# Performance work log

Measured on AMD Instinct MI355X. Metric: run time of the kernel, lower is better.

The kernel has to match this reference:

```python
import jax, jax.numpy as jnp
import numpy as np

N, E, FD, PD, C0, C1 = 50000, 1000000, 1024, 64, 64, 64


def setup_inputs() -> dict:
    key = jax.random.key(0)
    ks = iter(jax.random.split(key, 64))
    nrm = lambda s, sc=0.05: jax.random.normal(next(ks), s, jnp.float32) * sc

    def bn_p(c):
        # rows: gamma, beta, running_mean, running_var (eval-mode batchnorm)
        return jnp.stack([
            1.0 + 0.1 * jax.random.normal(next(ks), (c,)),
            0.1 * jax.random.normal(next(ks), (c,)),
            0.1 * jax.random.normal(next(ks), (c,)),
            0.5 + jax.random.uniform(next(ks), (c,)),
        ]).astype(jnp.float32)

    inp = {}
    inp["x"] = jax.random.normal(next(ks), (N, FD + 4), jnp.float32)
    inp["edge_index"] = jax.random.randint(next(ks), (2, E), 0, N, jnp.int32)
    inp["edge_attr"] = jax.random.randint(next(ks), (E,), 0, 3, jnp.int32) - 1  # {-1,0,1}
    inp["Wspf"] = nrm((PD, 4)); inp["bspf"] = nrm((PD,))
    inp["W011"] = nrm((C0, FD // 2 + PD)); inp["b011"] = nrm((C0,))
    inp["W012"] = nrm((C0, FD // 2)); inp["b012"] = nrm((C0,))
    inp["bn01"] = bn_p(C0)
    for i in (1, 2, 3):
        inp[f"e{i}W1"] = nrm((C0, 2 * C0)); inp[f"e{i}b1"] = nrm((C0,))
        inp[f"e{i}W2"] = nrm((C0, C0)); inp[f"e{i}b2"] = nrm((C0,))
        inp[f"bn1{i}"] = bn_p(C0)
    inp["s21Wl"] = nrm((C1, C0)); inp["s21bl"] = nrm((C1,)); inp["s21Wr"] = nrm((C1, C0))
    inp["bn21"] = bn_p(C1)
    for i in (1, 2, 3):
        inp[f"s3{i}Wl"] = nrm((1, C1)); inp[f"s3{i}bl"] = nrm((1,)); inp[f"s3{i}Wr"] = nrm((1, C1))
    return inp


def _bn(h, p):
    g, b, m, v = p
    return (h - m) * jax.lax.rsqrt(v + 1e-5) * g + b


def _edge_conv(h, src, dst, seg, n, W1, b1, W2, b2):
    # EdgeConv: max_j MLP([x_i, x_j - x_i]); masked edges routed to dummy segment n
    xi, xj = h[dst], h[src]
    msg = jax.nn.relu(jnp.concatenate([xi, xj - xi], axis=1) @ W1.T + b1) @ W2.T + b2
    out = jax.ops.segment_max(msg, seg, num_segments=n + 1)[:n]
    return jnp.where(jnp.isfinite(out), out, 0.0)  # nodes with no in-edges -> 0


def _sage(h, src, seg, n, Wl, bl, Wr):
    # SAGEConv: lin_l(mean_j x_j) + lin_r(x_i)
    s = jax.ops.segment_sum(h[src], seg, num_segments=n + 1)[:n]
    cnt = jax.ops.segment_sum(jnp.ones((seg.shape[0],), h.dtype), seg, num_segments=n + 1)[:n]
    agg = s / jnp.maximum(cnt, 1.0)[:, None]
    return agg @ Wl.T + bl + h @ Wr.T


def reference(x, edge_index, edge_attr, Wspf, bspf, W011, b011, W012, b012, bn01,
              e1W1, e1b1, e1W2, e1b2, bn11, e2W1, e2b1, e2W2, e2b2, bn12,
              e3W1, e3b1, e3W2, e3b2, bn13, s21Wl, s21bl, s21Wr, bn21,
              s31Wl, s31bl, s31Wr, s32Wl, s32bl, s32Wr, s33Wl, s33bl, s33Wr):
    fd = 1024
    n = x.shape[0]
    src, dst = edge_index[0], edge_index[1]
    seg1 = jnp.where(edge_attr >= 0, dst, n)  # forward-time edges
    seg2 = jnp.where(edge_attr <= 0, dst, n)  # backward-time edges
    seg3 = dst                                 # all edges

    spf = x[:, fd:fd + 4]
    x_vis = jnp.concatenate([x[:, fd // 2:fd], spf @ Wspf.T + bspf], axis=1) @ W011.T + b011
    x_aud = x[:, :fd // 2] @ W012.T + b012
    h = jax.nn.relu(_bn(x_aud + x_vis, bn01))

    def branch(eW1, eb1, eW2, eb2, bnE, seg, sWl, sbl, sWr):
        y = jax.nn.relu(_bn(_edge_conv(h, src, dst, seg, n, eW1, eb1, eW2, eb2), bnE))
        y = jax.nn.relu(_bn(_sage(y, src, seg, n, s21Wl, s21bl, s21Wr), bn21))
        return _sage(y, src, seg, n, sWl, sbl, sWr)

    o = (branch(e1W1, e1b1, e1W2, e1b2, bn11, seg1, s31Wl, s31bl, s31Wr)
         + branch(e2W1, e2b1, e2W2, e2b2, bn12, seg2, s32Wl, s32bl, s32Wr)
         + branch(e3W1, e3b1, e3W2, e3b2, bn13, seg3, s33Wl, s33bl, s33Wr))
    return jax.nn.sigmoid(o)
```

## Files before the change

### kernel.cpp

```cpp
#include <hip/hip_runtime.h>
#include <cstdint>
#include <cstddef>

#define NN 50000
#define EE 1000000
#define NBK 196
#define PW_EC 6144
#define PW_AG 8192
#define SG_PAD 136

typedef __attribute__((ext_vector_type(8))) short bf16x8;
typedef __attribute__((ext_vector_type(4))) short s16x4;
typedef __attribute__((ext_vector_type(4))) float f32x4;
typedef _Float16 f16;
typedef __attribute__((ext_vector_type(2))) _Float16 f16x2;
typedef __attribute__((ext_vector_type(4))) _Float16 f16x4;
typedef __attribute__((ext_vector_type(8))) _Float16 f16x8;

__device__ __forceinline__ void split2(float v, short& hi, short& lo) {
    union { float f; unsigned int u; } a; a.f = v;
    unsigned short h16 = (unsigned short)(a.u >> 16);
    union { unsigned int u; float f; } hf; hf.u = ((unsigned int)h16) << 16;
    union { float f; unsigned int u; } b; b.f = v - hf.f;
    hi = (short)h16;
    lo = (short)(b.u >> 16);
}

__device__ __forceinline__ f16x8 relupq(f16x8 p, f16x8 q) {
    f16x8 s = p + q;
    f16x8 z = {};
#if __has_builtin(__builtin_elementwise_max)
    return __builtin_elementwise_max(s, z);
#else
    f16x8 r;
#pragma unroll
    for (int j = 0; j < 8; j++) r[j] = (s[j] > (f16)0.f) ? s[j] : (f16)0.f;
    return r;
#endif
}

#define OFF_WHL    ((size_t)0)
#define OFF_WSPP   ((size_t)262144)
#define OFF_BIAS01 ((size_t)263168)
#define OFF_W1PQT  ((size_t)263424)
#define OFF_BIASPQ ((size_t)361728)
#define OFF_WSAGET ((size_t)363264)
#define OFF_BIAS21 ((size_t)396032)
#define OFF_BNF    ((size_t)396288)
#define OFF_W2BF   ((size_t)398848)
#define OFF_INVC4  ((size_t)423424)
#define OFF_PZ4    ((size_t)1223424)
#define OFF_RP     ((size_t)2023424)
#define OFF_PARTS  ((size_t)2223488)
#define OFF_DEG    ((size_t)2227584)
#define OFF_CNT01  ((size_t)2427648)
#define OFF_GHEAD  ((size_t)2627712)
#define OFF_SORT   ((size_t)2631808)
#define OFF_H      ((size_t)6631808)
#define OFF_PI     ((size_t)19431808)
#define OFF_QI     ((size_t)38631808)
#define OFF_Y1I    ((size_t)57831808)
#define OFF_EBUCK  OFF_H
#define OFF_AGGI   OFF_PI

__global__ __launch_bounds__(256) void k_prep(
    const float* __restrict__ Wspf, const float* __restrict__ bspf,
    const float* __restrict__ W011, const float* __restrict__ b011,
    const float* __restrict__ W012, const float* __restrict__ b012,
    const float* __restrict__ bn01,
    const float* __restrict__ e1W1, const float* __restrict__ e1b1,
    const float* __restrict__ e1b2, const float* __restrict__ bn11,
    const float* __restrict__ e2W1, const float* __restrict__ e2b1,
    const float* __restrict__ e2b2, const float* __restrict__ bn12,
    const float* __restrict__ e3W1, const float* __restrict__ e3b1,
    const float* __restrict__ e3b2, const float* __restrict__ bn13,
    const float* __restrict__ e1W2, const float* __restrict__ e2W2,
    const float* __restrict__ e3W2,
    const float* __restrict__ s21Wl, const float* __restrict__ s21bl,
    const float* __restrict__ s21Wr, const float* __restrict__ bn21,
    unsigned short* __restrict__ Whl, float* __restrict__ WspP, float* __restrict__ bias01,
    float* __restrict__ W1pqT, float* __restrict__ biasPQ,
    f16* __restrict__ Wsg16, float* __restrict__ bias21, float* __restrict__ bnf,
    f16* __restrict__ W2h)
{
    int idx = blockIdx.x * 256 + threadIdx.x;
    if (idx < 131072) {
        int hl = idx >> 16;
        int r = idx & 65535;
        int kchunk = r >> 11;
        int r2 = r & 2047;
        int blk = r2 >> 9;
        int r3 = r2 & 511;
        int lane = r3 >> 3;
        int j = r3 & 7;
        int n = lane & 15, quad = lane >> 4;
        int k = kchunk * 32 + quad * 8 + j;
        int c = blk * 16 + n;
        float s = bn01[c] * rsqrtf(bn01[192 + c] + 1e-5f);
        float w = ((k < 512) ? W012[c * 512 + k] : W011[c * 576 + (k - 512)]) * s;
        short hi, lo;
        split2(w, hi, lo);
        Whl[idx] = (unsigned short)(hl ? lo : hi);
    } else if (idx < 131072 + 24576) {
        int r = idx - 131072;
        int b = r >> 13; r &= 8191;
        int k = r >> 7, cp = r & 127;
        const float* W1 = (b == 0) ? e1W1 : (b == 1) ? e2W1 : e3W1;
        float val;
        if (cp < 64) val = W1[cp * 128 + k] - W1[cp * 128 + 64 + k];
        else         val = W1[(cp - 64) * 128 + 64 + k];
        W1pqT[b * 8192 + k * 128 + cp] = val;
    } else if (idx < 131072 + 24576 + 8192) {
        int r = idx - (131072 + 24576);
        int k = r >> 6, c = r & 63;
        float s = bn21[c] * rsqrtf(bn21[192 + c] + 1e-5f);
        float w = (k < 64) ? s21Wl[c * 64 + k] : s21Wr[c * 64 + (k - 64)];
        Wsg16[c * 128 + k] = (f16)(w * s);
    } else if (idx < 131072 + 24576 + 8192 + 64) {
        int c = idx - (131072 + 24576 + 8192);
        float s01 = bn01[c] * rsqrtf(bn01[192 + c] + 1e-5f);
        float wsp0 = 0.f, wsp1 = 0.f, wsp2 = 0.f, wsp3 = 0.f, bacc = 0.f;
        for (int j = 0; j < 64; j++) {
            float w = W011[c * 576 + 512 + j];
            wsp0 += w * Wspf[j * 4 + 0];
            wsp1 += w * Wspf[j * 4 + 1];
            wsp2 += w * Wspf[j * 4 + 2];
            wsp3 += w * Wspf[j * 4 + 3];
            bacc += w * bspf[j];
        }
        WspP[c * 4 + 0] = wsp0 * s01; WspP[c * 4 + 1] = wsp1 * s01;
        WspP[c * 4 + 2] = wsp2 * s01; WspP[c * 4 + 3] = wsp3 * s01;
        bias01[c] = (b011[c] + b012[c] + bacc) * s01 + (bn01[64 + c] - bn01[128 + c] * s01);
        float s21 = bn21[c] * rsqrtf(bn21[192 + c] + 1e-5f);
        bias21[c] = s21bl[c] * s21 + (bn21[64 + c] - bn21[128 + c] * s21);
        const float* b1a[3] = { e1b1, e2b1, e3b1 };
        const float* b2a[3] = { e1b2, e2b2, e3b2 };
        const float* bna[3] = { bn11, bn12, bn13 };
#pragma unroll
        for (int b = 0; b < 3; b++) {
            float s = bna[b][c] * rsqrtf(bna[b][192 + c] + 1e-5f);
            float tr = bna[b][64 + c] - bna[b][128 + c] * s;
            bnf[b * 192 + c] = s;
            bnf[b * 192 + 64 + c] = b2a[b][c] * s + tr;
            bnf[b * 192 + 128 + c] = tr;
            biasPQ[b * 128 + c] = b1a[b][c];
            biasPQ[b * 128 + 64 + c] = 0.f;
        }
    } else if (idx < 131072 + 24576 + 8192 + 64 + 12288) {
        int r = idx - (131072 + 24576 + 8192 + 64);
        int b = r >> 12, i = r & 4095;
        const float* W2 = (b == 0) ? e1W2 : (b == 1) ? e2W2 : e3W2;
        W2h[b * 4096 + i] = (f16)W2[i];
    }
}

__global__ __launch_bounds__(256) void k_hist(
    const int* __restrict__ dst, int* __restrict__ deg)
{
    int e = blockIdx.x * 256 + threadIdx.x;
    if (e < EE) atomicAdd(&deg[dst[e]], 1);
}

__global__ __launch_bounds__(256) void k_psum(const int* __restrict__ deg, int* __restrict__ parts)
{
    int i = blockIdx.x * 256 + threadIdx.x;
    int v = (i < NN) ? deg[i] : 0;
#pragma unroll
    for (int off = 32; off > 0; off >>= 1) v += __shfl_xor(v, off);
    __shared__ int ws4[4];
    int wid = threadIdx.x >> 6;
    if ((threadIdx.x & 63) == 0) ws4[wid] = v;
    __syncthreads();
    if (threadIdx.x == 0)
        parts[blockIdx.x] = ws4[0] + ws4[1] + ws4[2] + ws4[3];
}

__global__ __launch_bounds__(256) void k_pscan(int* __restrict__ parts, int* __restrict__ ghead)
{
    __shared__ int sbuf[256];
    int tid = threadIdx.x;
    int v = (tid < NBK) ? parts[tid] : 0;
    sbuf[tid] = v;
    __syncthreads();
    for (int off = 1; off < 256; off <<= 1) {
        int t = (tid >= off) ? sbuf[tid - off] : 0;
        __syncthreads();
        sbuf[tid] += t;
        __syncthreads();
    }
    if (tid < NBK) {
        int ex = sbuf[tid] - v;
        parts[tid] = ex;
        ghead[tid] = ex;
    }
}

__global__ __launch_bounds__(256) void k_scanfix(
    const int* __restrict__ deg, const int* __restrict__ parts, int* __restrict__ rowptr)
{
    __shared__ int sbuf[256];
    int tid = threadIdx.x;
    int i = blockIdx.x * 256 + tid;
    int v = (i < NN) ? deg[i] : 0;
    sbuf[tid] = v;
    __syncthreads();
    for (int off = 1; off < 256; off <<= 1) {
        int t = (tid >= off) ? sbuf[tid - off] : 0;
        __syncthreads();
        sbuf[tid] += t;
        __syncthreads();
    }
    int base = parts[blockIdx.x];
    if (i < NN)      rowptr[i] = base + sbuf[tid] - v;
    if (i == NN - 1) rowptr[NN] = base + sbuf[tid];
}

__global__ __launch_bounds__(256) void k_bucketA(
    const int* __restrict__ src, const int* __restrict__ dst, const int* __restrict__ attr,
    int* __restrict__ ghead, unsigned int* __restrict__ ebuck)
{
    __shared__ int hist[NBK];
    __shared__ int head[NBK];
    int tid = threadIdx.x;
    if (tid < NBK) hist[tid] = 0;
    __syncthreads();
    int base_e = blockIdx.x * 4096;
    unsigned int word[16]; int bkt[16];
#pragma unroll
    for (int k = 0; k < 16; k++) {
        int e = base_e + k * 256 + tid;
        if (e < EE) {
            int d = dst[e], s = src[e], a = attr[e] + 1;
            int b = d >> 8;
            word[k] = (unsigned)s | ((unsigned)a << 16) | ((unsigned)(d & 255) << 18);
            bkt[k] = b;
            atomicAdd(&hist[b], 1);
        } else { bkt[k] = -1; word[k] = 0; }
    }
    __syncthreads();
    if (tid < NBK) {
        int c = hist[tid];
        head[tid] = c ? atomicAdd(&ghead[tid], c) : 0;
    }
    __syncthreads();
#pragma unroll
    for (int k = 0; k < 16; k++) {
        if (bkt[k] >= 0) {
            int pos = atomicAdd(&head[bkt[k]], 1);
            ebuck[pos] = word[k];
        }
    }
}

__global__ __launch_bounds__(256) void k_bucketB(
    const int* __restrict__ rp, const unsigned int* __restrict__ ebuck,
    int* __restrict__ sorted, unsigned int* __restrict__ cnt01)
{
    __shared__ int sbuf[1024];
    __shared__ int head[1024];
    __shared__ int s2[256];
    int b = blockIdx.x, tid = threadIdx.x;
    int n0 = b * 256;
    int n1 = n0 + 256; if (n1 > NN) n1 = NN;
    int r0 = rp[n0];
    int r1 = rp[n1];
    for (int i = tid; i < 1024; i += 256) sbuf[i] = 0;
    __syncthreads();
    for (int e = r0 + tid; e < r1; e += 256)
        atomicAdd(&sbuf[(ebuck[e] >> 16) & 1023], 1);
    __syncthreads();
    int i0 = tid * 4;
    int v0 = sbuf[i0], v1 = sbuf[i0 + 1], v2 = sbuf[i0 + 2], v3 = sbuf[i0 + 3];
    if (n0 + tid < NN)
        cnt01[n0 + tid] = (unsigned)v0 | ((unsigned)v1 << 16);
    int tot = v0 + v1 + v2 + v3;
    s2[tid] = tot;
    __syncthreads();
    for (int off = 1; off < 256; off <<= 1) {
        int t = (tid >= off) ? s2[tid - off] : 0;
        __syncthreads();
        s2[tid] += t;
        __syncthreads();
    }
    int ex = s2[tid] - tot;
    head[i0]     = r0 + ex;
    head[i0 + 1] = r0 + ex + v0;
    head[i0 + 2] = r0 + ex + v0 + v1;
    head[i0 + 3] = r0 + ex + v0 + v1 + v2;
    __syncthreads();
    for (int e = r0 + tid; e < r1; e += 256) {
        unsigned int w = ebuck[e];
        int pos = atomicAdd(&head[(w >> 16) & 1023], 1);
        sorted[pos] = (int)(w & 0x3FFFFu);
    }
}

__global__ __launch_bounds__(256) void k_h(
    const float* __restrict__ x, const unsigned short* __restrict__ Whl,
    const float* __restrict__ WspP, const float* __restrict__ bias01,
    float* __restrict__ h)
{
    __shared__ unsigned short hib[2][4096];
    __shared__ unsigned short lob[2][4096];
    int tid = threadIdx.x;
    int w = tid >> 6, l = tid & 63;
    int tile = blockIdx.x;
    int m = l & 15, quad = l >> 4;
    int blk = w;
    const unsigned short* Wh = Whl;
    const unsigned short* Wl = Whl + 65536;
    const size_t xbase = (size_t)tile * 16 * 1028;

    int oct_w = l >> 1, off_w = (l & 1) * 4;

    f32x4 g[4];
#pragma unroll
    for (int p = 0; p < 4; p++)
        g[p] = *(const f32x4*)(x + xbase + (size_t)(p * 4 + w) * 1028 + l * 4);
#pragma unroll
    for (int p = 0; p < 4; p++) {
        int r = p * 4 + w;
        int op = r * 256 + (oct_w ^ (r & 7)) * 8 + off_w;
        s16x4 h4, l4;
#pragma unroll
        for (int i = 0; i < 4; i++) { short hi, lo; split2(g[p][i], hi, lo); h4[i] = hi; l4[i] = lo; }
        *(s16x4*)(&hib[0][op]) = h4;
        *(s16x4*)(&lob[0][op]) = l4;
    }
    __syncthreads();

    f32x4 acc = { 0.f, 0.f, 0.f, 0.f };
    for (int c = 0; c < 4; c++) {
        if (c < 3) {
#pragma unroll
            for (int p = 0; p < 4; p++)
                g[p] = *(const f32x4*)(x + xbase + (size_t)(p * 4 + w) * 1028 + (c + 1) * 256 + l * 4);
        }
        int buf = c & 1;
        const unsigned short* hp = &hib[buf][m * 256];
        const unsigned short* lp = &lob[buf][m * 256];
        int msw = m & 7;
#pragma unroll
        for (int ks = 0; ks < 8; ks++) {
            int oct = ks * 4 + quad;
            int ao = (oct ^ msw) * 8;
            bf16x8 xh = *(const bf16x8*)(hp + ao);
            bf16x8 xl = *(const bf16x8*)(lp + ao);
            int fb = (c * 8 + ks) * 2048 + blk * 512 + l * 8;
            bf16x8 bh = *(const bf16x8*)(Wh + fb);
            bf16x8 bl = *(const bf16x8*)(Wl + fb);
            acc = __builtin_amdgcn_mfma_f32_16x16x32_bf16(xh, bh, acc, 0, 0, 0);
            acc = __builtin_amdgcn_mfma_f32_16x16x32_bf16(xl, bh, acc, 0, 0, 0);
            acc = __builtin_amdgcn_mfma_f32_16x16x32_bf16(xh, bl, acc, 0, 0, 0);
        }
        if (c < 3) {
            int nbuf = (c + 1) & 1;
#pragma unroll
            for (int p = 0; p < 4; p++) {
                int r = p * 4 + w;
                int op = r * 256 + (oct_w ^ (r & 7)) * 8 + off_w;
                s16x4 h4, l4;
#pragma unroll
                for (int i = 0; i < 4; i++) { short hi, lo; split2(g[p][i], hi, lo); h4[i] = hi; l4[i] = lo; }
                *(s16x4*)(&hib[nbuf][op]) = h4;
                *(s16x4*)(&lob[nbuf][op]) = l4;
            }
            __syncthreads();
        }
    }

    int ch = blk * 16 + m;
    f32x4 wsp = *(const f32x4*)(WspP + ch * 4);
    float bia = bias01[ch];
#pragma unroll
    for (int r = 0; r < 4; r++) {
        int row = tile * 16 + quad * 4 + r;
        f32x4 sp = *(const f32x4*)(x + (size_t)row * 1028 + 1024);
        float a = acc[r] + sp[0] * wsp[0] + sp[1] * wsp[1]
                + sp[2] * wsp[2] + sp[3] * wsp[3] + bia;
        h[(size_t)row * 64 + ch] = fmaxf(a, 0.f);
    }
}

__global__ __launch_bounds__(256) void k_pq(
    const float* __restrict__ h, const float* __restrict__ WT3,
    const float* __restrict__ biasPQ, f16* __restrict__ Pi, f16* __restrict__ Qi)
{
    __shared__ float wt[64 * 128];
    __shared__ float xt[64 * 68];
    int tid = threadIdx.x;
    int m0 = blockIdx.x * 64;
    int cg = tid & 31, rg = tid >> 5;
#pragma unroll
    for (int i = 0; i < 4; i++) {
        int li = i * 256 + tid;
        int rr = li >> 4, q = li & 15;
        int row = m0 + rr;
        float4 u = make_float4(0.f, 0.f, 0.f, 0.f);
        if (row < NN) u = *(const float4*)(h + (size_t)row * 64 + q * 4);
        *(float4*)(xt + rr * 68 + q * 4) = u;
    }
    for (int b = 0; b < 3; b++) {
        __syncthreads();
#pragma unroll
        for (int i = 0; i < 8; i++)
            ((float4*)wt)[i * 256 + tid] = ((const float4*)(WT3 + b * 8192))[i * 256 + tid];
        __syncthreads();
        float acc[8][4];
#pragma unroll
        for (int r = 0; r < 8; r++)
#pragma unroll
            for (int j = 0; j < 4; j++) acc[r][j] = 0.f;
#pragma unroll 8
        for (int k = 0; k < 64; k++) {
            float4 wv = *(const float4*)(wt + k * 128 + cg * 4);
#pragma unroll
            for (int r = 0; r < 8; r++) {
                float xv = xt[(rg * 8 + r) * 68 + k];
                acc[r][0] += xv * wv.x; acc[r][1] += xv * wv.y;
                acc[r][2] += xv * wv.z; acc[r][3] += xv * wv.w;
            }
        }
        const float* biasP = biasPQ + b * 128;
#pragma unroll
        for (int r = 0; r < 8; r++) {
            int row = m0 + rg * 8 + r;
            if (row < NN) {
                if (cg < 16) {
                    f16x4 res;
#pragma unroll
                    for (int j = 0; j < 4; j++)
                        res[j] = (f16)(acc[r][j] + biasP[cg * 4 + j]);
                    *(f16x4*)(Pi + (size_t)row * 192 + b * 64 + cg * 4) = res;
                } else {
                    f16x4 res;
#pragma unroll
                    for (int j = 0; j < 4; j++)
                        res[j] = (f16)acc[r][j];
                    *(f16x4*)(Qi + (size_t)row * 192 + b * 64 + (cg - 16) * 4) = res;
                }
            }
        }
    }
}

#define ECV_BRANCH(B, EST, ECN)                                                    \
    {                                                                              \
        f16x8 pl = *(const f16x8*)(pr + (B) * 64 + quad * 8);                      \
        f16x8 ph = *(const f16x8*)(pr + (B) * 64 + 32 + quad * 8);                 \
        float acc[4][4];                                                           \
        _Pragma("unroll") for (int blk = 0; blk < 4; blk++)                        \
            _Pragma("unroll") for (int r = 0; r < 4; r++) acc[blk][r] = -3.0e38f;  \
        int nbF = (ECN) >> 4;                                                      \
        int rem = (ECN) & 15;                                                      \
        for (int bi = 0; bi < nbF; bi++) {                                         \
            int srcm = sorted[(EST) + bi * 16 + m] & 0xFFFF;                       \
            const f16* qr = Qi + (size_t)srcm * 192 + (B) * 64;                    \
            f16x8 q0 = *(const f16x8*)(qr + quad * 8);                             \
            f16x8 q1 = *(const f16x8*)(qr + 32 + quad * 8);                        \
            f16x8 a0 = relupq(pl, q0);                                             \
            f16x8 a1 = relupq(ph, q1);                                             \
            _Pragma("unroll") for (int blk = 0; blk < 4; blk++) {                  \
                f32x4 c = { 0.f, 0.f, 0.f, 0.f };                                  \
                f16x8 w0 = *(const f16x8*)(w2s + ((B) * 8 + blk * 2 + 0) * 512 + quad * 128 + m * 8); \
                f16x8 w1 = *(const f16x8*)(w2s + ((B) * 8 + blk * 2 + 1) * 512 + quad * 128 + m * 8); \
                c = __builtin_amdgcn_mfma_f32_16x16x32_f16(a0, w0, c, 0, 0, 0);    \
                c = __builtin_amdgcn_mfma_f32_16x16x32_f16(a1, w1, c, 0, 0, 0);    \
                _Pragma("unroll") for (int r = 0; r < 4; r++)                      \
                    acc[blk][r] = fmaxf(acc[blk][r], c[r]);                        \
            }                                                                      \
        }                                                                          \
        if (rem) {                                                                 \
            int e = (EST) + nbF * 16 + m;                                          \
            int srcm = sorted[(m < rem) ? e : (EST)] & 0xFFFF;                     \
            const f16* qr = Qi + (size_t)srcm * 192 + (B) * 64;                    \
            f16x8 q0 = *(const f16x8*)(qr + quad * 8);                             \
            f16x8 q1 = *(const f16x8*)(qr + 32 + quad * 8);                        \
            f16x8 a0 = relupq(pl, q0);                                             \
            f16x8 a1 = relupq(ph, q1);                                             \
            _Pragma("unroll") for (int blk = 0; blk < 4; blk++) {                  \
                f32x4 c = { 0.f, 0.f, 0.f, 0.f };                                  \
                f16x8 w0 = *(const f16x8*)(w2s + ((B) * 8 + blk * 2 + 0) * 512 + quad * 128 + m * 8); \
                f16x8 w1 = *(const f16x8*)(w2s + ((B) * 8 + blk * 2 + 1) * 512 + quad * 128 + m * 8); \
                c = __builtin_amdgcn_mfma_f32_16x16x32_f16(a0, w0, c, 0, 0, 0);    \
                c = __builtin_amdgcn_mfma_f32_16x16x32_f16(a1, w1, c, 0, 0, 0);    \
                _Pragma("unroll") for (int r = 0; r < 4; r++)                      \
                    if (quad * 4 + r < rem)                                        \
                        acc[blk][r] = fmaxf(acc[blk][r], c[r]);                    \
            }                                                                      \
        }                                                                          \
        float red[4];                                                              \
        _Pragma("unroll") for (int blk = 0; blk < 4; blk++) {                      \
            float rv = fmaxf(fmaxf(acc[blk][0], acc[blk][1]),                      \
                             fmaxf(acc[blk][2], acc[blk][3]));                     \
            rv = fmaxf(rv, __shfl_xor(rv, 16));                                    \
            rv = fmaxf(rv, __shfl_xor(rv, 32));                                    \
            red[blk] = rv;                                                         \
        }                                                                          \
        float mx = red[quad];                                                      \
        const float* scb = bnf + (B) * 192;                                        \
        float outv = ((ECN) > 0) ? fmaxf(fmaf(mx, scb[lane], scb[64 + lane]), 0.f) \
                                 : fmaxf(scb[128 + lane], 0.f);                    \
        y1i[(size_t)v * 192 + (B) * 64 + lane] = (f16)outv;                        \
    }

__global__ __launch_bounds__(256) void k_edgeconv_f(
    const int* __restrict__ rowptr, const unsigned int* __restrict__ cnt01,
    const int* __restrict__ sorted,
    const f16* __restrict__ Pi, const f16* __restrict__ Qi,
    const f16* __restrict__ W2h,
    const float* __restrict__ bnf,
    f16* __restrict__ y1i, float* __restrict__ invc4)
{
    __shared__ f16 w2s[12288];
    int tid = threadIdx.x;
#pragma unroll
    for (int u0 = 0; u0 < 6; u0++) {
        int u = u0 * 256 + tid;
        int frag = u >> 6;
        int rem = u & 63;
        int m2 = rem >> 2, qd = rem & 3;
        int bb = frag >> 3, blk = (frag >> 1) & 3, kc = frag & 1;
        *(int4*)(w2s + frag * 512 + qd * 128 + m2 * 8) =
            *(const int4*)(W2h + (bb * 64 + blk * 16 + m2) * 64 + kc * 32 + qd * 8);
    }
    __syncthreads();

    int wid = tid >> 6, lane = tid & 63;
    int m = lane & 15, quad = lane >> 4;
    int gw = blockIdx.x * 4 + wid;

    for (int v = gw; v < NN; v += PW_EC) {
        const f16* pr = Pi + (size_t)v * 192;
        int e0 = rowptr[v], e1 = rowptr[v + 1];
        int deg = e1 - e0;
        unsigned int cc = cnt01[v];
        int c0 = (int)(cc & 0xFFFFu);
        int c1 = (int)(cc >> 16);
        int n1cnt = deg - c0;
        int n2cnt = c0 + c1;

        ECV_BRANCH(0, e0 + c0, n1cnt)
        ECV_BRANCH(1, e0, n2cnt)
        ECV_BRANCH(2, e0, deg)

        if (lane == 0) {
            float4 ic;
            ic.x = 1.f / (float)(n1cnt > 0 ? n1cnt : 1);
            ic.y = 1.f / (float)(n2cnt > 0 ? n2cnt : 1);
            ic.z = 1.f / (float)(deg   > 0 ? deg   : 1);
            ic.w = 0.f;
            *(float4*)(invc4 + (size_t)v * 4) = ic;
        }
    }
}

#define AGG_BRANCH(B, EST, ECN, ICS)                                               \
    {                                                                              \
        float s[8];                                                                \
        _Pragma("unroll") for (int j = 0; j < 8; j++) s[j] = 0.f;                  \
        for (int eb = 0; eb < (ECN); eb += 8) {                                    \
            if (eb + eslot < (ECN)) {                                              \
                int src = sorted[(EST) + eb + eslot] & 0xFFFF;                     \
                f16x8 u = *(const f16x8*)(y1i + (size_t)src * 192 + (B) * 64 + cg * 8); \
                _Pragma("unroll") for (int j = 0; j < 8; j++) s[j] += (float)u[j]; \
            }                                                                      \
        }                                                                          \
        _Pragma("unroll") for (int j = 0; j < 8; j++) {                            \
            s[j] += __shfl_xor(s[j], 8);                                           \
            s[j] += __shfl_xor(s[j], 16);                                          \
            s[j] += __shfl_xor(s[j], 32);                                          \
        }                                                                          \
        if (eslot == 0) {                                                          \
            f16x8 r;                                                               \
            _Pragma("unroll") for (int j = 0; j < 8; j++) r[j] = (f16)(s[j] * (ICS)); \
            *(f16x8*)(aggi + (size_t)v * 192 + (B) * 64 + cg * 8) = r;             \
        }                                                                          \
    }

__global__ __launch_bounds__(256) void k_agg_f(
    const int* __restrict__ rowptr, const unsigned int* __restrict__ cnt01,
    const int* __restrict__ sorted,
    const f16* __restrict__ y1i, const float* __restrict__ invc4,
    f16* __restrict__ aggi)
{
    int wid = threadIdx.x >> 6, lane = threadIdx.x & 63;
    int eslot = lane >> 3, cg = lane & 7;
    int gw = blockIdx.x * 4 + wid;
    for (int v = gw; v < NN; v += PW_AG) {
        int e0 = rowptr[v], e1 = rowptr[v + 1];
        int deg = e1 - e0;
        unsigned int cc = cnt01[v];
        int c0 = (int)(cc & 0xFFFFu);
        int c1 = (int)(cc >> 16);
        float4 icv = *(const float4*)(invc4 + (size_t)v * 4);
        AGG_BRANCH(0, e0 + c0, deg - c0, icv.x)
        AGG_BRANCH(1, e0, c0 + c1, icv.y)
        AGG_BRANCH(2, e0, deg, icv.z)
    }
}

__global__ __launch_bounds__(256) void k_sage1(
    const f16* __restrict__ aggi, const f16* __restrict__ y1i,
    const f16* __restrict__ Wsg16,
    const float* __restrict__ bias21,
    const float* __restrict__ Wl0, const float* __restrict__ bl0, const float* __restrict__ Wr0,
    const float* __restrict__ Wl1, const float* __restrict__ bl1, const float* __restrict__ Wr1,
    const float* __restrict__ Wl2, const float* __restrict__ bl2, const float* __restrict__ Wr2,
    float* __restrict__ pz4)
{
    __shared__ f16 wsg[64 * SG_PAD];
    int tid = threadIdx.x;
    for (int i = tid; i < 1024; i += 256) {
        int c = i >> 4, kq = i & 15;
        *(f16x8*)(wsg + c * SG_PAD + kq * 8) = *(const f16x8*)(Wsg16 + c * 128 + kq * 8);
    }
    __syncthreads();

    int wid = tid >> 6, lane = tid & 63;
    int m = lane & 15, quad = lane >> 4;
    int tile = blockIdx.x * 4 + wid;
    if (tile >= 3125) return;
    int rowm = tile * 16 + m;
    int rowq = tile * 16 + quad * 4;

    const float* Wlp[3] = { Wl0, Wl1, Wl2 };
    const float* Wrp[3] = { Wr0, Wr1, Wr2 };
    const float* blp[3] = { bl0, bl1, bl2 };

    float zsum[4] = { 0.f, 0.f, 0.f, 0.f };
#pragma unroll
    for (int b = 0; b < 3; b++) {
        const f16* ra = aggi + (size_t)rowm * 192 + b * 64 + quad * 8;
        const f16* ry = y1i  + (size_t)rowm * 192 + b * 64 + quad * 8;
        f16x8 a0 = *(const f16x8*)(ra);
        f16x8 a1 = *(const f16x8*)(ra + 32);
        f16x8 a2 = *(const f16x8*)(ry);
        f16x8 a3 = *(const f16x8*)(ry + 32);
        float ps[4] = { 0.f, 0.f, 0.f, 0.f };
        float zs[4] = { 0.f, 0.f, 0.f, 0.f };
#pragma unroll
        for (int cb = 0; cb < 4; cb++) {
            int col = cb * 16 + m;
            const f16* wb = wsg + col * SG_PAD + quad * 8;
            f32x4 acc = { 0.f, 0.f, 0.f, 0.f };
            acc = __builtin_amdgcn_mfma_f32_16x16x32_f16(a0, *(const f16x8*)(wb),      acc, 0, 0, 0);
            acc = __builtin_amdgcn_mfma_f32_16x16x32_f16(a1, *(const f16x8*)(wb + 32), acc, 0, 0, 0);
            acc = __builtin_amdgcn_mfma_f32_16x16x32_f16(a2, *(const f16x8*)(wb + 64), acc, 0, 0, 0);
            acc = __builtin_amdgcn_mfma_f32_16x16x32_f16(a3, *(const f16x8*)(wb + 96), acc, 0, 0, 0);
            float bz = bias21[col];
            float wlv = Wlp[b][col];
            float wrv = Wrp[b][col];
#pragma unroll
            for (int r = 0; r < 4; r++) {
                float y = fmaxf(acc[r] + bz, 0.f);
                ps[r] += y * wlv;
                zs[r] += y * wrv;
            }
        }
        float blv = blp[b][0];
#pragma unroll
        for (int r = 0; r < 4; r++) {
            ps[r] += __shfl_xor(ps[r], 1); ps[r] += __shfl_xor(ps[r], 2);
            ps[r] += __shfl_xor(ps[r], 4); ps[r] += __shfl_xor(ps[r], 8);
            zs[r] += __shfl_xor(zs[r], 1); zs[r] += __shfl_xor(zs[r], 2);
            zs[r] += __shfl_xor(zs[r], 4); zs[r] += __shfl_xor(zs[r], 8);
            zsum[r] += zs[r] + blv;
        }
        if (m == 0) {
#pragma unroll
            for (int r = 0; r < 4; r++)
                pz4[(size_t)(rowq + r) * 4 + b] = ps[r];
        }
    }
    if (m == 0) {
#pragma unroll
        for (int r = 0; r < 4; r++)
            pz4[(size_t)(rowq + r) * 4 + 3] = zsum[r];
    }
}

__global__ __launch_bounds__(256) void k_sage2_f(
    const int* __restrict__ rowptr, const int* __restrict__ sorted,
    const float* __restrict__ pz4, const float* __restrict__ invc4,
    float* __restrict__ outp)
{
    int wid = threadIdx.x >> 6, lane = threadIdx.x & 63;
    int sub = lane >> 4, sl = lane & 15;
    int gw = blockIdx.x * 4 + wid;
    for (int v = gw * 4 + sub; v < NN; v += PW_AG * 4) {
        int e0 = rowptr[v], e1 = rowptr[v + 1];
        float s1 = 0.f, s2 = 0.f, s3 = 0.f;
        for (int e = e0 + sl; e < e1; e += 16) {
            int w = sorted[e];
            int src = w & 0xFFFF, a = (w >> 16) & 3;
            float4 pz = *(const float4*)(pz4 + (size_t)src * 4);
            s3 += pz.z;
            if (a >= 1) s1 += pz.x;
            if (a <= 1) s2 += pz.y;
        }
#pragma unroll
        for (int off = 1; off < 16; off <<= 1) {
            s1 += __shfl_xor(s1, off);
            s2 += __shfl_xor(s2, off);
            s3 += __shfl_xor(s3, off);
        }
        if (sl == 0) {
            float4 icv = *(const float4*)(invc4 + (size_t)v * 4);
            float zsum = pz4[(size_t)v * 4 + 3];
            float val = s1 * icv.x + s2 * icv.y + s3 * icv.z + zsum;
            outp[v] = 1.f / (1.f + expf(-val));
        }
    }
}

extern "C" void kernel_launch(void* const* d_in, const int* in_sizes, int n_in,
                              void* d_out, int out_size, void* d_ws, size_t ws_size,
                              hipStream_t stream)
{
    const float* x    = (const float*)d_in[0];
    const int* ei     = (const int*)d_in[1];
    const int* attr   = (const int*)d_in[2];
    const float* Wspf = (const float*)d_in[3];
    const float* bspf = (const float*)d_in[4];
    const float* W011 = (const float*)d_in[5];
    const float* b011 = (const float*)d_in[6];
    const float* W012 = (const float*)d_in[7];
    const float* b012 = (const float*)d_in[8];
    const float* bn01 = (const float*)d_in[9];
    const float* eW1[3] = { (const float*)d_in[10], (const float*)d_in[15], (const float*)d_in[20] };
    const float* eb1[3] = { (const float*)d_in[11], (const float*)d_in[16], (const float*)d_in[21] };
    const float* eW2[3] = { (const float*)d_in[12], (const float*)d_in[17], (const float*)d_in[22] };
    const float* eb2[3] = { (const float*)d_in[13], (const float*)d_in[18], (const float*)d_in[23] };
    const float* bn1[3] = { (const float*)d_in[14], (const float*)d_in[19], (const float*)d_in[24] };
    const float* s21Wl = (const float*)d_in[25];
    const float* s21bl = (const float*)d_in[26];
    const float* s21Wr = (const float*)d_in[27];
    const float* bn21  = (const float*)d_in[28];
    const float* s3Wl[3] = { (const float*)d_in[29], (const float*)d_in[32], (const float*)d_in[35] };
    const float* s3bl[3] = { (const float*)d_in[30], (const float*)d_in[33], (const float*)d_in[36] };
    const float* s3Wr[3] = { (const float*)d_in[31], (const float*)d_in[34], (const float*)d_in[37] };

    char* ws = (char*)d_ws;
    unsigned short* Whl = (unsigned short*)(ws + OFF_WHL);
    float* WspP   = (float*)(ws + OFF_WSPP);
    float* bias01 = (float*)(ws + OFF_BIAS01);
    float* W1pqT  = (float*)(ws + OFF_W1PQT);
    float* biasPQ = (float*)(ws + OFF_BIASPQ);
    f16*   Wsg16  = (f16*)(ws + OFF_WSAGET);
    float* bias21 = (float*)(ws + OFF_BIAS21);
    float* bnf    = (float*)(ws + OFF_BNF);
    f16*   W2h    = (f16*)(ws + OFF_W2BF);
    float* invc4  = (float*)(ws + OFF_INVC4);
    float* pz4    = (float*)(ws + OFF_PZ4);
    int*   rp     = (int*)(ws + OFF_RP);
    int*   parts  = (int*)(ws + OFF_PARTS);
    int*   deg    = (int*)(ws + OFF_DEG);
    unsigned int* cnt01 = (unsigned int*)(ws + OFF_CNT01);
    int*   ghead  = (int*)(ws + OFF_GHEAD);
    int*   sorted = (int*)(ws + OFF_SORT);
    unsigned int* ebuck = (unsigned int*)(ws + OFF_EBUCK);
    float* h      = (float*)(ws + OFF_H);
    f16*   Pi     = (f16*)(ws + OFF_PI);
    f16*   Qi     = (f16*)(ws + OFF_QI);
    f16*   y1i    = (f16*)(ws + OFF_Y1I);
    f16*   aggi   = (f16*)(ws + OFF_AGGI);

    hipMemsetAsync(ws + OFF_DEG, 0, 200064, stream);

    k_prep<<<689, 256, 0, stream>>>(
        Wspf, bspf, W011, b011, W012, b012, bn01,
        eW1[0], eb1[0], eb2[0], bn1[0],
        eW1[1], eb1[1], eb2[1], bn1[1],
        eW1[2], eb1[2], eb2[2], bn1[2],
        eW2[0], eW2[1], eW2[2],
        s21Wl, s21bl, s21Wr, bn21,
        Whl, WspP, bias01, W1pqT, biasPQ, Wsg16, bias21, bnf, W2h);

    k_hist<<<3907, 256, 0, stream>>>(ei + EE, deg);
    k_psum<<<NBK, 256, 0, stream>>>(deg, parts);
    k_pscan<<<1, 256, 0, stream>>>(parts, ghead);
    k_scanfix<<<NBK, 256, 0, stream>>>(deg, parts, rp);
    k_bucketA<<<245, 256, 0, stream>>>(ei, ei + EE, attr, ghead, ebuck);
    k_bucketB<<<NBK, 256, 0, stream>>>(rp, ebuck, sorted, cnt01);

    k_h<<<3125, 256, 0, stream>>>(x, Whl, WspP, bias01, h);

    k_pq<<<782, 256, 0, stream>>>(h, W1pqT, biasPQ, Pi, Qi);

    k_edgeconv_f<<<PW_EC / 4, 256, 0, stream>>>(rp, cnt01, sorted, Pi, Qi, W2h, bnf, y1i, invc4);
    k_agg_f<<<PW_AG / 4, 256, 0, stream>>>(rp, cnt01, sorted, y1i, invc4, aggi);

    k_sage1<<<782, 256, 0, stream>>>(aggi, y1i, Wsg16, bias21,
                                     s3Wl[0], s3bl[0], s3Wr[0],
                                     s3Wl[1], s3bl[1], s3Wr[1],
                                     s3Wl[2], s3bl[2], s3Wr[2], pz4);

    k_sage2_f<<<PW_AG / 4, 256, 0, stream>>>(rp, sorted, pz4, invc4, (float*)d_out);
}
```

Before: 711.4 us.

## Compute P/Q projection with fp16 MFMA and store h in fp16

The P/Q projection kernel used to be an fp32 shared-memory SIMT GEMM. It now runs on 16x16x32 f16 MFMA instructions, with each wave handling a 16-row tile and reading A and B fragments directly from global memory. The node features h are written as fp16 instead of fp32, which halves their storage and read traffic, and the W1 weights are prepacked transposed in fp16. The cost is lower precision for h and the weights in this projection, plus scattered 2-byte output stores.

```diff
diff --git a/kernel.cpp b/kernel.cpp
--- a/kernel.cpp
+++ b/kernel.cpp
@@ -79,7 +79,7 @@
     const float* __restrict__ s21Wl, const float* __restrict__ s21bl,
     const float* __restrict__ s21Wr, const float* __restrict__ bn21,
     unsigned short* __restrict__ Whl, float* __restrict__ WspP, float* __restrict__ bias01,
-    float* __restrict__ W1pqT, float* __restrict__ biasPQ,
+    f16* __restrict__ W1h, float* __restrict__ biasPQ,
     f16* __restrict__ Wsg16, float* __restrict__ bias21, float* __restrict__ bnf,
     f16* __restrict__ W2h)
 {
@@ -109,7 +109,7 @@
         float val;
         if (cp < 64) val = W1[cp * 128 + k] - W1[cp * 128 + 64 + k];
         else         val = W1[(cp - 64) * 128 + 64 + k];
-        W1pqT[b * 8192 + k * 128 + cp] = val;
+        W1h[b * 8192 + cp * 64 + k] = (f16)val;
     } else if (idx < 131072 + 24576 + 8192) {
         int r = idx - (131072 + 24576);
         int k = r >> 6, c = r & 63;
@@ -298,7 +298,7 @@
 __global__ __launch_bounds__(256) void k_h(
     const float* __restrict__ x, const unsigned short* __restrict__ Whl,
     const float* __restrict__ WspP, const float* __restrict__ bias01,
-    float* __restrict__ h)
+    f16* __restrict__ h)
 {
     __shared__ unsigned short hib[2][4096];
     __shared__ unsigned short lob[2][4096];
@@ -378,67 +378,45 @@
         f32x4 sp = *(const f32x4*)(x + (size_t)row * 1028 + 1024);
         float a = acc[r] + sp[0] * wsp[0] + sp[1] * wsp[1]
                 + sp[2] * wsp[2] + sp[3] * wsp[3] + bia;
-        h[(size_t)row * 64 + ch] = fmaxf(a, 0.f);
+        h[(size_t)row * 64 + ch] = (f16)fmaxf(a, 0.f);
     }
 }
 
 __global__ __launch_bounds__(256) void k_pq(
-    const float* __restrict__ h, const float* __restrict__ WT3,
+    const f16* __restrict__ h, const f16* __restrict__ W1h,
     const float* __restrict__ biasPQ, f16* __restrict__ Pi, f16* __restrict__ Qi)
 {
-    __shared__ float wt[64 * 128];
-    __shared__ float xt[64 * 68];
     int tid = threadIdx.x;
-    int m0 = blockIdx.x * 64;
-    int cg = tid & 31, rg = tid >> 5;
-#pragma unroll
-    for (int i = 0; i < 4; i++) {
-        int li = i * 256 + tid;
-        int rr = li >> 4, q = li & 15;
-        int row = m0 + rr;
-        float4 u = make_float4(0.f, 0.f, 0.f, 0.f);
-        if (row < NN) u = *(const float4*)(h + (size_t)row * 64 + q * 4);
-        *(float4*)(xt + rr * 68 + q * 4) = u;
-    }
+    int wid = tid >> 6, lane = tid & 63;
+    int m = lane & 15, quad = lane >> 4;
+    int tile = blockIdx.x * 4 + wid;
+    if (tile >= 3125) return;
+    int rowm = tile * 16 + m;
+    int rowq = tile * 16 + quad * 4;
+
+    const f16* hr = h + (size_t)rowm * 64 + quad * 8;
+    f16x8 a0 = *(const f16x8*)(hr);
+    f16x8 a1 = *(const f16x8*)(hr + 32);
+
+#pragma unroll
     for (int b = 0; b < 3; b++) {
-        __syncthreads();
-#pragma unroll
-        for (int i = 0; i < 8; i++)
-            ((float4*)wt)[i * 256 + tid] = ((const float4*)(WT3 + b * 8192))[i * 256 + tid];
-        __syncthreads();
-        float acc[8][4];
-#pragma unroll
-        for (int r = 0; r < 8; r++)
-#pragma unroll
-            for (int j = 0; j < 4; j++) acc[r][j] = 0.f;
-#pragma unroll 8
-        for (int k = 0; k < 64; k++) {
-            float4 wv = *(const float4*)(wt + k * 128 + cg * 4);
-#pragma unroll
-            for (int r = 0; r < 8; r++) {
-                float xv = xt[(rg * 8 + r) * 68 + k];
-                acc[r][0] += xv * wv.x; acc[r][1] += xv * wv.y;
-                acc[r][2] += xv * wv.z; acc[r][3] += xv * wv.w;
-            }
-        }
-        const float* biasP = biasPQ + b * 128;
-#pragma unroll
-        for (int r = 0; r < 8; r++) {
-            int row = m0 + rg * 8 + r;
-            if (row < NN) {
-                if (cg < 16) {
-                    f16x4 res;
-#pragma unroll
-                    for (int j = 0; j < 4; j++)
-                        res[j] = (f16)(acc[r][j] + biasP[cg * 4 + j]);
-                    *(f16x4*)(Pi + (size_t)row * 192 + b * 64 + cg * 4) = res;
-                } else {
-                    f16x4 res;
-#pragma unroll
-                    for (int j = 0; j < 4; j++)
-                        res[j] = (f16)acc[r][j];
-                    *(f16x4*)(Qi + (size_t)row * 192 + b * 64 + (cg - 16) * 4) = res;
-                }
+        const f16* wb0 = W1h + b * 8192;
+#pragma unroll
+        for (int cb = 0; cb < 8; cb++) {
+            int col = cb * 16 + m;
+            const f16* wbp = wb0 + col * 64 + quad * 8;
+            f32x4 acc = { 0.f, 0.f, 0.f, 0.f };
+            acc = __builtin_amdgcn_mfma_f32_16x16x32_f16(a0, *(const f16x8*)(wbp),      acc, 0, 0, 0);
+            acc = __builtin_amdgcn_mfma_f32_16x16x32_f16(a1, *(const f16x8*)(wbp + 32), acc, 0, 0, 0);
+            if (cb < 4) {
+                float bz = biasPQ[b * 128 + col];
+#pragma unroll
+                for (int r = 0; r < 4; r++)
+                    Pi[(size_t)(rowq + r) * 192 + b * 64 + col] = (f16)(acc[r] + bz);
+            } else {
+#pragma unroll
+                for (int r = 0; r < 4; r++)
+                    Qi[(size_t)(rowq + r) * 192 + b * 64 + (col - 64)] = (f16)acc[r];
             }
         }
     }
@@ -745,7 +723,7 @@
     unsigned short* Whl = (unsigned short*)(ws + OFF_WHL);
     float* WspP   = (float*)(ws + OFF_WSPP);
     float* bias01 = (float*)(ws + OFF_BIAS01);
-    float* W1pqT  = (float*)(ws + OFF_W1PQT);
+    f16*   W1h    = (f16*)(ws + OFF_W1PQT);
     float* biasPQ = (float*)(ws + OFF_BIASPQ);
     f16*   Wsg16  = (f16*)(ws + OFF_WSAGET);
     float* bias21 = (float*)(ws + OFF_BIAS21);
@@ -760,7 +738,7 @@
     int*   ghead  = (int*)(ws + OFF_GHEAD);
     int*   sorted = (int*)(ws + OFF_SORT);
     unsigned int* ebuck = (unsigned int*)(ws + OFF_EBUCK);
-    float* h      = (float*)(ws + OFF_H);
+    f16*   h16    = (f16*)(ws + OFF_H);
     f16*   Pi     = (f16*)(ws + OFF_PI);
     f16*   Qi     = (f16*)(ws + OFF_QI);
     f16*   y1i    = (f16*)(ws + OFF_Y1I);
@@ -775,7 +753,7 @@
         eW1[2], eb1[2], eb2[2], bn1[2],
         eW2[0], eW2[1], eW2[2],
         s21Wl, s21bl, s21Wr, bn21,
-        Whl, WspP, bias01, W1pqT, biasPQ, Wsg16, bias21, bnf, W2h);
+        Whl, WspP, bias01, W1h, biasPQ, Wsg16, bias21, bnf, W2h);
 
     k_hist<<<3907, 256, 0, stream>>>(ei + EE, deg);
     k_psum<<<NBK, 256, 0, stream>>>(deg, parts);
@@ -784,9 +762,9 @@
     k_bucketA<<<245, 256, 0, stream>>>(ei, ei + EE, attr, ghead, ebuck);
     k_bucketB<<<NBK, 256, 0, stream>>>(rp, ebuck, sorted, cnt01);
 
-    k_h<<<3125, 256, 0, stream>>>(x, Whl, WspP, bias01, h);
-
-    k_pq<<<782, 256, 0, stream>>>(h, W1pqT, biasPQ, Pi, Qi);
+    k_h<<<3125, 256, 0, stream>>>(x, Whl, WspP, bias01, h16);
+
+    k_pq<<<782, 256, 0, stream>>>(h16, W1h, biasPQ, Pi, Qi);
 
     k_edgeconv_f<<<PW_EC / 4, 256, 0, stream>>>(rp, cnt01, sorted, Pi, Qi, W2h, bnf, y1i, invc4);
     k_agg_f<<<PW_AG / 4, 256, 0, stream>>>(rp, cnt01, sorted, y1i, invc4, aggi);
```

Result: faster. 684.7 us (-3.7%).
